# Kernel tuning notes

Hardware: AMD Instinct MI355X
Metric: run time of the kernel (lower is better)

The kernel has to match this reference:

```python
import jax, jax.numpy as jnp
import numpy as np

N, M, E = 20000, 5000, 320000   # nodes, hyperedges, incidence edges
HEADS, OUT, EDIM = 4, 32, 32
NEG_SLOPE = 0.2


def setup_inputs() -> dict:
    key = jax.random.key(0)
    ks = jax.random.split(key, 7)
    feat = jax.random.normal(ks[0], (N, HEADS * OUT), jnp.float32)
    edge_feat = jax.random.normal(ks[1], (E, EDIM), jnp.float32)
    H = jax.random.uniform(ks[2], (N, M), jnp.float32)
    attn_l = jax.random.normal(ks[3], (1, HEADS, OUT), jnp.float32)
    attn_m = jax.random.normal(ks[4], (1, HEADS, EDIM), jnp.float32)
    src = jax.random.randint(ks[5], (E,), 0, N, jnp.int32)
    dst = jax.random.randint(ks[6], (E,), 0, M, jnp.int32)
    return dict(feat=feat, edge_feat=edge_feat, H=H,
                attn_l=attn_l, attn_m=attn_m, src=src, dst=dst)


def _segment_softmax(e, seg, num):
    # numerically stable softmax over edges grouped by destination segment
    emax = jax.ops.segment_max(e, seg, num_segments=num)
    emax = jnp.where(jnp.isfinite(emax), emax, 0.0)  # guard empty segments
    ex = jnp.exp(e - emax[seg])
    den = jax.ops.segment_sum(ex, seg, num_segments=num)
    return ex / den[seg]


def reference(feat, edge_feat, H, attn_l, attn_m, src, dst):
    feat_src = feat.reshape(-1, HEADS, OUT)                 # [N,h,d]
    el = (feat_src * attn_l).sum(-1)                        # [N,h]
    em = (edge_feat[:, None, :] * attn_m).sum(-1)           # [E,h]
    e = el[src] + em                                        # [E,h]
    e = jnp.where(e > 0, e, NEG_SLOPE * e)                  # LeakyReLU
    a = _segment_softmax(e, dst, M)                         # edge softmax per dst
    msg = feat_src[src] * a[..., None]                      # [E,h,d]
    agg = jax.ops.segment_sum(msg, dst, num_segments=M)     # [M,h,d]
    rst = jnp.einsum('nm,mdk->ndk', H, agg)                 # [N,h,d]
    return rst.reshape(rst.shape[0], -1)
```

## Files before the change

### kernel.cpp

```cpp
#include <hip/hip_runtime.h>

#define NN 20000
#define MM 5000
#define EE 320000
#define FD 128
#define KD 5000
#define K2 5120
#define NEG 0.2f
#define BK 128
#define BUFB 65536
#define BOFF 32768
#define NKT 40
#define SPLITK 4
#define KTPS 10
#define PS4 640000

typedef __attribute__((ext_vector_type(4))) float f32x4;
typedef __attribute__((ext_vector_type(8))) short short8;

__device__ __forceinline__ unsigned int f2bf(float x){
  unsigned int u = __float_as_uint(x);
  return (u + 0x7fffu + ((u >> 16) & 1u)) >> 16;
}
__device__ __forceinline__ unsigned int cvtpk(float lo, float hi){
  unsigned int r;
  asm volatile("v_cvt_pk_bf16_f32 %0, %1, %2" : "=v"(r) : "v"(lo), "v"(hi));
  return r;
}
__device__ __forceinline__ void dma16(const void* g, void* l){
  __builtin_amdgcn_global_load_lds(
      (const __attribute__((address_space(1))) void*)g,
      (__attribute__((address_space(3))) void*)l, 16, 0, 0);
}

__global__ __launch_bounds__(256) void k_el(const float* __restrict__ feat,
                                            const float* __restrict__ attn_l,
                                            float* __restrict__ el){
  int t = threadIdx.x;
  int node = blockIdx.x*4 + (t>>6);
  int l = t & 63;
  float2 f = ((const float2*)feat)[(size_t)node*64 + l];
  float p = f.x*attn_l[2*l] + f.y*attn_l[2*l+1];
  p += __shfl_xor(p,1); p += __shfl_xor(p,2); p += __shfl_xor(p,4); p += __shfl_xor(p,8);
  if ((l&15)==0) el[node*4 + (l>>4)] = p;
}

__global__ __launch_bounds__(256) void k_edge(const float* __restrict__ edge_feat,
                                              const float* __restrict__ attn_m,
                                              const float* __restrict__ el,
                                              const int* __restrict__ src,
                                              const int* __restrict__ dst,
                                              int* __restrict__ counts,
                                              float4* __restrict__ e4){
  __shared__ float am[128];
  int t = threadIdx.x;
  if (t < 128) am[t] = attn_m[t];
  __syncthreads();
  int e = blockIdx.x*16 + (t>>4);
  int c = t & 15;
  float2 f = ((const float2*)edge_feat)[(size_t)e*16 + c];
  float p0 = f.x*am[0*32+2*c] + f.y*am[0*32+2*c+1];
  float p1 = f.x*am[1*32+2*c] + f.y*am[1*32+2*c+1];
  float p2 = f.x*am[2*32+2*c] + f.y*am[2*32+2*c+1];
  float p3 = f.x*am[3*32+2*c] + f.y*am[3*32+2*c+1];
  #pragma unroll
  for (int s=1; s<16; s<<=1){
    p0 += __shfl_xor(p0,s); p1 += __shfl_xor(p1,s);
    p2 += __shfl_xor(p2,s); p3 += __shfl_xor(p3,s);
  }
  if (c==0){
    float4 ev = ((const float4*)el)[src[e]];
    float4 r;
    float v;
    v = ev.x + p0; r.x = v > 0.f ? v : NEG*v;
    v = ev.y + p1; r.y = v > 0.f ? v : NEG*v;
    v = ev.z + p2; r.z = v > 0.f ? v : NEG*v;
    v = ev.w + p3; r.w = v > 0.f ? v : NEG*v;
    e4[e] = r;
    atomicAdd(&counts[dst[e]], 1);
  }
}

__global__ __launch_bounds__(256) void k_scan(const int* __restrict__ counts,
                                              int* __restrict__ offsets){
  __shared__ int sc[256];
  int t = threadIdx.x;
  int loc[20];
  int sum = 0;
  #pragma unroll
  for (int j=0;j<20;j++){
    int idx = t*20 + j;
    int v = (idx < MM) ? counts[idx] : 0;
    loc[j] = sum; sum += v;
  }
  sc[t] = sum; __syncthreads();
  for (int s=1; s<256; s<<=1){
    int v = 0;
    if (t >= s) v = sc[t-s];
    __syncthreads();
    if (t >= s) sc[t] += v;
    __syncthreads();
  }
  int base = sc[t] - sum;
  #pragma unroll
  for (int j=0;j<20;j++){
    int idx = t*20 + j;
    if (idx < MM) offsets[idx] = base + loc[j];
  }
  if (t == 250) offsets[MM] = base;
}

__global__ __launch_bounds__(256) void k_scatter(const int* __restrict__ dst,
                                                 const int* __restrict__ offsets,
                                                 int* __restrict__ cursor,
                                                 int* __restrict__ edge_ids){
  int e = blockIdx.x*256 + threadIdx.x;
  if (e < EE){
    int d = dst[e];
    int pos = atomicAdd(&cursor[d], 1);
    edge_ids[offsets[d] + pos] = e;
  }
}

__global__ __launch_bounds__(256) void k_agg(const float4* __restrict__ e4,
                                             const float* __restrict__ feat,
                                             const int* __restrict__ src,
                                             const int* __restrict__ edge_ids,
                                             const int* __restrict__ offsets,
                                             unsigned short* __restrict__ aggT){
  int m = blockIdx.x;
  int t = threadIdx.x;
  if (m < (K2 - KD) && t < FD) aggT[(size_t)t*K2 + KD + m] = 0;
  int beg = offsets[m], end = offsets[m+1];
  int cnt = end - beg;
  if (cnt == 0){
    if (t < FD) aggT[(size_t)t*K2 + m] = 0;
    return;
  }
  __shared__ float accs[4][FD];
  __shared__ float dens[4][4];
  int w = t>>6, l = t&63, h = l>>4;
  float accx=0.f, accy=0.f, den=0.f;
  const float2* feat2 = (const float2*)feat;
  for (int i=w; i<cnt; i+=4){
    int eid = edge_ids[beg+i];
    float4 ev = e4[eid];
    float eh = (h==0)?ev.x:((h==1)?ev.y:((h==2)?ev.z:ev.w));
    float p = __expf(eh - 32.0f);
    float2 f = feat2[(size_t)src[eid]*64 + l];
    accx += p*f.x; accy += p*f.y; den += p;
  }
  accs[w][2*l]   = accx;
  accs[w][2*l+1] = accy;
  if ((l&15)==0) dens[w][h] = den;
  __syncthreads();
  if (t < FD){
    float s = accs[0][t]+accs[1][t]+accs[2][t]+accs[3][t];
    float dn = dens[0][t>>5]+dens[1][t>>5]+dens[2][t>>5]+dens[3][t>>5];
    aggT[(size_t)t*K2 + m] = (unsigned short)f2bf(s/dn);
  }
}

__global__ __launch_bounds__(512, 2) void k_gemm(const float* __restrict__ H,
                                                 const unsigned short* __restrict__ aggT,
                                                 float* __restrict__ part){
  __shared__ char lds[2*BUFB];
  int t = threadIdx.x;
  int row0 = blockIdx.x * 64;
  int kt0 = blockIdx.y * KTPS;

  int w8 = t>>6, l = t&63;
  const size_t AMAX = (size_t)NN*KD - 4;

  int wr = (w8>>2)*32, wc = (w8&3)*32;
  int rl = l&15, kg = l>>4;
  int arowA = (wr+rl)*512;
  int arowB = (wr+16+rl)*512;
  int bcol0 = BOFF + (wc+ 0+rl)*256;
  int bcol1 = BOFF + (wc+16+rl)*256;

  f32x4 acc00={0,0,0,0}, acc01={0,0,0,0};
  f32x4 acc10={0,0,0,0}, acc11={0,0,0,0};

#define STAGE(KT, BUF)                                                        \
  { size_t kb_ = (size_t)(KT)*BK;                                             \
    _Pragma("unroll")                                                         \
    for (int j=0;j<4;j++){                \
      int r_ = row0 + w8*8 + j*2 + (l>>5);                                    \
      if (r_ > NN-1) r_ = NN-1;                                               \
      size_t s_ = (size_t)r_*KD + (size_t)((l&31) ^ (r_&15))*4 + kb_;         \
      if (s_ > AMAX) s_ = AMAX;                                               \
      dma16(H + s_, (BUF) + (w8*8 + j*2)*512);                                \
    }                                                                         \
    _Pragma("unroll")                                                         \
    for (int j=0;j<4;j++){                \
      int c_ = w8*16 + j*4 + (l>>4);                                          \
      size_t s_ = (size_t)c_*K2 + (size_t)((l&15) ^ (c_&15))*8 + kb_;         \
      dma16(aggT + s_, (BUF) + BOFF + (w8*16 + j*4)*256);                     \
    }                                                                         \
  }

#define COMP_KK(R_, KK)                                                       \
  { int gA0 = (KK)*8 + kg*2;                                                  \
    int sA0 = ((gA0  ) ^ rl) << 4;                                            \
    int sA1 = ((gA0+1) ^ rl) << 4;                                            \
    f32x4 x0_ = *(const f32x4*)(R_ + arowA + sA0);                            \
    f32x4 x1_ = *(const f32x4*)(R_ + arowA + sA1);                            \
    f32x4 y0_ = *(const f32x4*)(R_ + arowB + sA0);                            \
    f32x4 y1_ = *(const f32x4*)(R_ + arowB + sA1);                            \
    int sB_ = (((KK)*4 + kg) ^ rl) << 4;                                      \
    short8 b0_ = *(const short8*)(R_ + bcol0 + sB_);                          \
    short8 b1_ = *(const short8*)(R_ + bcol1 + sB_);                          \
    uint4 ua_, ub_;                                                           \
    ua_.x = cvtpk(x0_[0],x0_[1]); ua_.y = cvtpk(x0_[2],x0_[3]);               \
    ua_.z = cvtpk(x1_[0],x1_[1]); ua_.w = cvtpk(x1_[2],x1_[3]);               \
    ub_.x = cvtpk(y0_[0],y0_[1]); ub_.y = cvtpk(y0_[2],y0_[3]);               \
    ub_.z = cvtpk(y1_[0],y1_[1]); ub_.w = cvtpk(y1_[2],y1_[3]);               \
    short8 a0_ = *(short8*)&ua_;                                              \
    short8 a1_ = *(short8*)&ub_;                                              \
    acc00 = __builtin_amdgcn_mfma_f32_16x16x32_bf16(a0_,b0_,acc00,0,0,0);     \
    acc01 = __builtin_amdgcn_mfma_f32_16x16x32_bf16(a0_,b1_,acc01,0,0,0);     \
    acc10 = __builtin_amdgcn_mfma_f32_16x16x32_bf16(a1_,b0_,acc10,0,0,0);     \
    acc11 = __builtin_amdgcn_mfma_f32_16x16x32_bf16(a1_,b1_,acc11,0,0,0);     \
  }

  STAGE(kt0,   lds)
  STAGE(kt0+1, lds + BUFB)

  int pr = 0;
  for (int tt = 0; tt < KTPS; ++tt){
    if (tt+1 < KTPS) { asm volatile("s_waitcnt vmcnt(8)" ::: "memory"); }
    else             { asm volatile("s_waitcnt vmcnt(0)" ::: "memory"); }
    __builtin_amdgcn_s_barrier();
    { const char* R_ = lds + pr*BUFB;
      COMP_KK(R_, 0)
      COMP_KK(R_, 1)
      COMP_KK(R_, 2)
      COMP_KK(R_, 3)
    }
    __builtin_amdgcn_s_barrier();
    __builtin_amdgcn_sched_barrier(0);
    if (tt+2 < KTPS) STAGE(kt0+tt+2, lds + pr*BUFB)
    pr ^= 1;
  }
#undef STAGE
#undef COMP_KK

  float* pout = part + (size_t)blockIdx.y*NN*FD;
#define STORE(ACC, FR, FN)                                                    \
  { _Pragma("unroll")                                                         \
    for (int q=0;q<4;q++){                                                    \
      int r = row0 + wr + (FR)*16 + kg*4 + q;                                 \
      if (r < NN) pout[(size_t)r*FD + wc + (FN)*16 + rl] = ACC[q];            \
    } }
  STORE(acc00,0,0) STORE(acc01,0,1)
  STORE(acc10,1,0) STORE(acc11,1,1)
#undef STORE
}

__global__ __launch_bounds__(256) void k_reduce(const float4* __restrict__ part,
                                                float4* __restrict__ out){
  int i = blockIdx.x*256 + threadIdx.x;
  float4 a = part[i];
  float4 b = part[i + 1*PS4];
  float4 c = part[i + 2*PS4];
  float4 d = part[i + 3*PS4];
  float4 r;
  r.x = (a.x+b.x)+(c.x+d.x);
  r.y = (a.y+b.y)+(c.y+d.y);
  r.z = (a.z+b.z)+(c.z+d.z);
  r.w = (a.w+b.w)+(c.w+d.w);
  out[i] = r;
}

extern "C" void kernel_launch(void* const* d_in, const int* in_sizes, int n_in,
                              void* d_out, int out_size, void* d_ws, size_t ws_size,
                              hipStream_t stream) {
  const float* feat      = (const float*)d_in[0];
  const float* edge_feat = (const float*)d_in[1];
  const float* H         = (const float*)d_in[2];
  const float* attn_l    = (const float*)d_in[3];
  const float* attn_m    = (const float*)d_in[4];
  const int*   src       = (const int*)d_in[5];
  const int*   dst       = (const int*)d_in[6];
  float* out = (float*)d_out;

  char* w = (char*)d_ws;
  float*          el       = (float*)(w + 0);
  unsigned short* aggT     = (unsigned short*)(w + 0);
  float4*         e4       = (float4*)(w + 1310720);
  int*            counts   = (int*)(w + 6430720);
  int*            cursor   = (int*)(w + 6451200);
  int*            offsets  = (int*)(w + 6471680);
  int*            edge_ids = (int*)(w + 6492160);
  float*          part     = (float*)(w + 7772160);

  hipMemsetAsync(counts, 0, 2*20480, stream);

  k_el     <<<NN/4,   256, 0, stream>>>(feat, attn_l, el);
  k_edge   <<<EE/16,  256, 0, stream>>>(edge_feat, attn_m, el, src, dst, counts, e4);
  k_scan   <<<1,      256, 0, stream>>>(counts, offsets);
  k_scatter<<<EE/256, 256, 0, stream>>>(dst, offsets, cursor, edge_ids);
  k_agg    <<<MM,     256, 0, stream>>>(e4, feat, src, edge_ids, offsets, aggT);
  k_gemm   <<<dim3((NN+63)/64, SPLITK), 512, 0, stream>>>(H, aggT, part);
  k_reduce <<<PS4/256, 256, 0, stream>>>((const float4*)part, (float4*)out);
}
```

Measured before the change: 247.1 us.

## Sort edge data by destination in scatter and gather bf16 features in aggregation

The scatter kernel now writes src and e4 values directly into destination-sorted arrays instead of edge ids, which removes a level of indirection in the aggregation loop. A new kernel converts feat to packed bf16 so the per-edge feature gather moves half the bytes. The aggregation loop is unrolled by two to keep more gathers in flight. The cost is an extra conversion kernel, more workspace, a larger scatter write, and bf16 rounding of the features used in aggregation.

```diff
diff --git a/kernel.cpp b/kernel.cpp
--- a/kernel.cpp
+++ b/kernel.cpp
@@ -45,6 +45,16 @@
   if ((l&15)==0) el[node*4 + (l>>4)] = p;
 }
 
+__global__ __launch_bounds__(256) void k_feat16(const float4* __restrict__ feat,
+                                                uint4* __restrict__ fb){
+  int i = blockIdx.x*256 + threadIdx.x;
+  float4 a = feat[2*i], b = feat[2*i+1];
+  uint4 r;
+  r.x = cvtpk(a.x,a.y); r.y = cvtpk(a.z,a.w);
+  r.z = cvtpk(b.x,b.y); r.w = cvtpk(b.z,b.w);
+  fb[i] = r;
+}
+
 __global__ __launch_bounds__(256) void k_edge(const float* __restrict__ edge_feat,
                                               const float* __restrict__ attn_m,
                                               const float* __restrict__ el,
@@ -111,21 +121,24 @@
 }
 
 __global__ __launch_bounds__(256) void k_scatter(const int* __restrict__ dst,
+                                                 const int* __restrict__ src,
+                                                 const float4* __restrict__ e4,
                                                  const int* __restrict__ offsets,
                                                  int* __restrict__ cursor,
-                                                 int* __restrict__ edge_ids){
+                                                 int* __restrict__ src_s,
+                                                 float4* __restrict__ e4_s){
   int e = blockIdx.x*256 + threadIdx.x;
   if (e < EE){
     int d = dst[e];
-    int pos = atomicAdd(&cursor[d], 1);
-    edge_ids[offsets[d] + pos] = e;
-  }
-}
-
-__global__ __launch_bounds__(256) void k_agg(const float4* __restrict__ e4,
-                                             const float* __restrict__ feat,
-                                             const int* __restrict__ src,
-                                             const int* __restrict__ edge_ids,
+    int pos = offsets[d] + atomicAdd(&cursor[d], 1);
+    src_s[pos] = src[e];
+    e4_s[pos] = e4[e];
+  }
+}
+
+__global__ __launch_bounds__(256) void k_agg(const float4* __restrict__ e4_s,
+                                             const int* __restrict__ src_s,
+                                             const unsigned int* __restrict__ fb,
                                              const int* __restrict__ offsets,
                                              unsigned short* __restrict__ aggT){
   int m = blockIdx.x;
@@ -141,14 +154,32 @@
   __shared__ float dens[4][4];
   int w = t>>6, l = t&63, h = l>>4;
   float accx=0.f, accy=0.f, den=0.f;
-  const float2* feat2 = (const float2*)feat;
-  for (int i=w; i<cnt; i+=4){
-    int eid = edge_ids[beg+i];
-    float4 ev = e4[eid];
+  int i = w;
+  #pragma unroll 1
+  for (; i+4 < cnt; i += 8){
+    float4 ev0 = e4_s[beg+i];
+    float4 ev1 = e4_s[beg+i+4];
+    int s0 = src_s[beg+i];
+    int s1 = src_s[beg+i+4];
+    unsigned int v0 = fb[(size_t)s0*64 + l];
+    unsigned int v1 = fb[(size_t)s1*64 + l];
+    float eh0 = (h==0)?ev0.x:((h==1)?ev0.y:((h==2)?ev0.z:ev0.w));
+    float eh1 = (h==0)?ev1.x:((h==1)?ev1.y:((h==2)?ev1.z:ev1.w));
+    float p0 = __expf(eh0 - 32.0f);
+    float p1 = __expf(eh1 - 32.0f);
+    accx += p0*__uint_as_float(v0<<16) + p1*__uint_as_float(v1<<16);
+    accy += p0*__uint_as_float(v0&0xffff0000u) + p1*__uint_as_float(v1&0xffff0000u);
+    den  += p0 + p1;
+  }
+  if (i < cnt){
+    float4 ev = e4_s[beg+i];
+    int s0 = src_s[beg+i];
+    unsigned int v = fb[(size_t)s0*64 + l];
     float eh = (h==0)?ev.x:((h==1)?ev.y:((h==2)?ev.z:ev.w));
     float p = __expf(eh - 32.0f);
-    float2 f = feat2[(size_t)src[eid]*64 + l];
-    accx += p*f.x; accy += p*f.y; den += p;
+    accx += p*__uint_as_float(v<<16);
+    accy += p*__uint_as_float(v&0xffff0000u);
+    den  += p;
   }
   accs[w][2*l]   = accx;
   accs[w][2*l+1] = accy;
@@ -292,16 +323,19 @@
   int*            counts   = (int*)(w + 6430720);
   int*            cursor   = (int*)(w + 6451200);
   int*            offsets  = (int*)(w + 6471680);
-  int*            edge_ids = (int*)(w + 6492160);
-  float*          part     = (float*)(w + 7772160);
+  int*            src_s    = (int*)(w + 6492160);
+  float4*         e4_s     = (float4*)(w + 7772160);
+  unsigned int*   fb       = (unsigned int*)(w + 12892160);
+  float*          part     = (float*)(w + 18012160);
 
   hipMemsetAsync(counts, 0, 2*20480, stream);
 
+  k_feat16 <<<1250,   256, 0, stream>>>((const float4*)feat, (uint4*)fb);
   k_el     <<<NN/4,   256, 0, stream>>>(feat, attn_l, el);
   k_edge   <<<EE/16,  256, 0, stream>>>(edge_feat, attn_m, el, src, dst, counts, e4);
   k_scan   <<<1,      256, 0, stream>>>(counts, offsets);
-  k_scatter<<<EE/256, 256, 0, stream>>>(dst, offsets, cursor, edge_ids);
-  k_agg    <<<MM,     256, 0, stream>>>(e4, feat, src, edge_ids, offsets, aggT);
+  k_scatter<<<EE/256, 256, 0, stream>>>(dst, src, e4, offsets, cursor, src_s, e4_s);
+  k_agg    <<<MM,     256, 0, stream>>>(e4_s, src_s, fb, offsets, aggT);
   k_gemm   <<<dim3((NN+63)/64, SPLITK), 512, 0, stream>>>(H, aggT, part);
   k_reduce <<<PS4/256, 256, 0, stream>>>((const float4*)part, (float4*)out);
 }
```

Result: faster. 216.9 us (-12.2%).
